# Performance work log

Measured on AMD Instinct MI355X. Metric: run time of the kernel, lower is better.

Reference implementation:

```python
import jax, jax.numpy as jnp
import numpy as np

QK_SCALE = 10.0  # fixed scale used with qk_norm (x-transformers/zeta default)
NEG_INF = -1e9


def layernorm(x, g, b, eps=1e-5):
    mu = jnp.mean(x, axis=-1, keepdims=True)
    var = jnp.var(x, axis=-1, keepdims=True)
    return (x - mu) * jax.lax.rsqrt(var + eps) * g + b


def l2norm(x, eps=1e-12):
    return x / jnp.sqrt(jnp.sum(x * x, axis=-1, keepdims=True) + eps)


def setup_inputs() -> dict:
    key = jax.random.key(0)
    ks = jax.random.split(key, 10)
    B, S, D, H, DH, E, FF = 2, 1024, 1024, 16, 64, 8, 4096
    sd = lambda fan: 1.0 / np.sqrt(fan)
    return {
        'x': jax.random.normal(ks[0], (B, S, D), jnp.float32),
        'ln_g': jnp.ones((D,), jnp.float32),
        'ln_b': jnp.zeros((D,), jnp.float32),
        'Wq': jax.random.normal(ks[1], (D, H * DH), jnp.float32) * sd(D),
        'Wk': jax.random.normal(ks[2], (D, H * DH), jnp.float32) * sd(D),
        'Wv': jax.random.normal(ks[3], (D, H * DH), jnp.float32) * sd(D),
        'q_scale': jnp.ones((H, 1, DH), jnp.float32),
        'k_scale': jnp.ones((H, 1, DH), jnp.float32),
        'Wo': jax.random.normal(ks[4], (H * DH, D), jnp.float32) * sd(H * DH),
        'gate_w': jax.random.normal(ks[5], (D, E), jnp.float32) * sd(D),
        'gate_b': jnp.zeros((E,), jnp.float32),
        'w1': jax.random.normal(ks[6], (E, D, FF), jnp.float32) * sd(D),
        'b1': jnp.zeros((E, FF), jnp.float32),
        'w2': jax.random.normal(ks[7], (E, FF, D), jnp.float32) * sd(FF),
        'b2': jnp.zeros((E, D), jnp.float32),
    }


def reference(x, ln_g, ln_b, Wq, Wk, Wv, q_scale, k_scale, Wo,
              gate_w, gate_b, w1, b1, w2, b2):
    B, S, D = x.shape
    H = q_scale.shape[0]
    DH = q_scale.shape[-1]

    # pre-attention LayerNorm (shared params)
    h = layernorm(x, ln_g, ln_b)

    # qk-normed causal multi-head attention
    q = (h @ Wq).reshape(B, S, H, DH).transpose(0, 2, 1, 3)  # b h s d
    k = (h @ Wk).reshape(B, S, H, DH).transpose(0, 2, 1, 3)
    v = (h @ Wv).reshape(B, S, H, DH).transpose(0, 2, 1, 3)
    q = l2norm(q) * q_scale
    k = l2norm(k) * k_scale
    logits = jnp.einsum('bhid,bhjd->bhij', q, k) * QK_SCALE
    causal = jnp.tril(jnp.ones((S, S), bool))
    logits = jnp.where(causal, logits, NEG_INF)
    attn = jax.nn.softmax(logits, axis=-1)
    out = jnp.einsum('bhij,bhjd->bhid', attn, v)
    out = out.transpose(0, 2, 1, 3).reshape(B, S, H * DH) @ Wo

    # mid LayerNorm (same shared params)
    h = layernorm(out, ln_g, ln_b)

    # SimpleMoE: softmax gate, dense combine over all experts
    gate = jax.nn.softmax(h @ gate_w + gate_b, axis=-1)  # b s e
    hid = jax.nn.gelu(jnp.einsum('bsd,edf->bsef', h, w1) + b1)  # b s e ff
    exp_out = jnp.einsum('bsef,efd->bsed', hid, w2) + b2  # b s e d
    moe = jnp.einsum('bse,bsed->bsd', gate, exp_out)

    # final LayerNorm (same shared params)
    return layernorm(moe, ln_g, ln_b)
```

## Files before the change

kernel.cpp:

```cpp
#include <hip/hip_runtime.h>

typedef unsigned short u16;
typedef float f32x4 __attribute__((ext_vector_type(4)));
typedef short short8 __attribute__((ext_vector_type(8)));

#define QK_SCALE_F 10.0f

#define GLD_LDS(g, l) __builtin_amdgcn_global_load_lds( \
    (const __attribute__((address_space(1))) unsigned int*)(g), \
    (__attribute__((address_space(3))) unsigned int*)(l), 16, 0, 0)

__device__ __forceinline__ u16 f2b(float f) {
  union { float f; unsigned u; } c; c.f = f;
  return (u16)((c.u + 0x7fffu + ((c.u >> 16) & 1u)) >> 16);
}

__device__ __forceinline__ float wred_sum(float v) {
#pragma unroll
  for (int m = 32; m > 0; m >>= 1) v += __shfl_xor(v, m, 64);
  return v;
}
__device__ __forceinline__ float wred_max(float v) {
#pragma unroll
  for (int m = 32; m > 0; m >>= 1) v = fmaxf(v, __shfl_xor(v, m, 64));
  return v;
}

#define BM 128
#define BN 128
#define BKK 64

template<int EPI>
__global__ __launch_bounds__(256)
void gemm_bt(const u16* __restrict__ A, const u16* __restrict__ B, void* __restrict__ Cv,
             int M, int N, int K, int lda, int ldb, int ldc,
             long zA, long zB, long zC,
             const float* __restrict__ P1, long zP1, const float* __restrict__ P2,
             int causal) {
  int z = blockIdx.z;
  int row0 = blockIdx.y * BM;
  int col0 = blockIdx.x * BN;
  if (causal && col0 > row0 + (BM - 1)) return;
  A += zA * z; B += zB * z;
  int tid = threadIdx.x;
  int wave = tid >> 6, lane = tid & 63;
  int wm = wave >> 1, wn = wave & 1;

  __shared__ __align__(16) u16 lA[2][BM * BKK];
  __shared__ __align__(16) u16 lB[2][BN * BKK];

  f32x4 acc[4][4];
  f32x4 zf = {0.f, 0.f, 0.f, 0.f};
#pragma unroll
  for (int i = 0; i < 4; i++)
#pragma unroll
    for (int j = 0; j < 4; j++) acc[i][j] = zf;

  int l3 = lane >> 3;
  int scol = ((lane & 7) ^ l3) << 3;
  long aoff[4], boff[4];
  int cbase[4];
#pragma unroll
  for (int i = 0; i < 4; i++) {
    int c = (wave << 2) + i;
    int r = (c << 3) + l3;
    aoff[i] = (long)(row0 + r) * lda + scol;
    boff[i] = (long)(col0 + r) * ldb + scol;
    cbase[i] = c << 10;
  }

  auto stage = [&](int buf, int k0) {
#pragma unroll
    for (int i = 0; i < 4; i++) {
      GLD_LDS(A + aoff[i] + k0, (char*)lA[buf] + cbase[i]);
      GLD_LDS(B + boff[i] + k0, (char*)lB[buf] + cbase[i]);
    }
  };

  int nt = K / BKK;
  stage(0, 0);
  int cur = 0;
  for (int t = 0; t < nt; ++t) {
    __syncthreads();
    if (t + 1 < nt) stage(cur ^ 1, (t + 1) * BKK);
    const char* pA = (const char*)lA[cur];
    const char* pB = (const char*)lB[cur];
#pragma unroll
    for (int kk = 0; kk < 2; kk++) {
      short8 af[4], bfr[4];
      int cb = (kk << 6) | ((lane >> 4) << 4);
#pragma unroll
      for (int mi = 0; mi < 4; mi++) {
        int R = (wm << 6) + (mi << 4) + (lane & 15);
        af[mi] = *(const short8*)(pA + ((R << 7) | (cb ^ ((R & 7) << 4))));
      }
#pragma unroll
      for (int nj = 0; nj < 4; nj++) {
        int R = (wn << 6) + (nj << 4) + (lane & 15);
        bfr[nj] = *(const short8*)(pB + ((R << 7) | (cb ^ ((R & 7) << 4))));
      }
#pragma unroll
      for (int mi = 0; mi < 4; mi++)
#pragma unroll
        for (int nj = 0; nj < 4; nj++)
          acc[mi][nj] = __builtin_amdgcn_mfma_f32_16x16x32_bf16(af[mi], bfr[nj], acc[mi][nj], 0, 0, 0);
    }
    cur ^= 1;
  }

#pragma unroll
  for (int mi = 0; mi < 4; mi++) {
#pragma unroll
    for (int nj = 0; nj < 4; nj++) {
#pragma unroll
      for (int rr = 0; rr < 4; rr++) {
        int row = row0 + (wm << 6) + (mi << 4) + ((lane >> 4) << 2) + rr;
        int col = col0 + (wn << 6) + (nj << 4) + (lane & 15);
        if (col < N) {
          float v = acc[mi][nj][rr];
          long cidx = zC * z + (long)row * ldc + col;
          if (EPI == 0) {
            ((float*)Cv)[cidx] = v;
          } else if (EPI == 2) {
            float t = v + P1[zP1 * z + col];
            float zz = 1.5957691216f * (t + 0.044715f * t * t * t);
            float gl = t / (1.f + __expf(-zz));
            ((u16*)Cv)[cidx] = f2b(gl * P2[((long)row << 3) + z]);
          }
        }
      }
    }
  }
}

__global__ __launch_bounds__(256)
void transpose_cast(const float* __restrict__ src, u16* __restrict__ dst,
                    int R, int C, long sz, long dz) {
  int z = blockIdx.z;
  src += sz * z; dst += dz * z;
  __shared__ float t[32][33];
  int c0 = blockIdx.x * 32, r0 = blockIdx.y * 32;
  int tx = threadIdx.x & 31, ty = threadIdx.x >> 5;
#pragma unroll
  for (int j = 0; j < 4; j++) {
    int r = ty + j * 8;
    t[r][tx] = src[(long)(r0 + r) * C + c0 + tx];
  }
  __syncthreads();
#pragma unroll
  for (int j = 0; j < 4; j++) {
    int r = ty + j * 8;
    dst[(long)(c0 + r) * R + r0 + tx] = f2b(t[tx][r]);
  }
}

__global__ __launch_bounds__(256)
void ln_kernel(const float* __restrict__ x, const float* __restrict__ g,
               const float* __restrict__ b, float* __restrict__ yf, u16* __restrict__ yb) {
  int tid = threadIdx.x;
  long base = (long)blockIdx.x << 10;
  float4 v = *(const float4*)&x[base + tid * 4];
  float s = v.x + v.y + v.z + v.w;
  float q = v.x * v.x + v.y * v.y + v.z * v.z + v.w * v.w;
  s = wred_sum(s); q = wred_sum(q);
  __shared__ float2 red[4];
  int wave = tid >> 6, lane = tid & 63;
  if (lane == 0) red[wave] = make_float2(s, q);
  __syncthreads();
  float S1 = red[0].x + red[1].x + red[2].x + red[3].x;
  float S2 = red[0].y + red[1].y + red[2].y + red[3].y;
  float mu = S1 * (1.f / 1024.f);
  float var = S2 * (1.f / 1024.f) - mu * mu;
  float rs = rsqrtf(var + 1e-5f);
  float4 gv = *(const float4*)&g[tid * 4];
  float4 bv = *(const float4*)&b[tid * 4];
  float4 o;
  o.x = (v.x - mu) * rs * gv.x + bv.x;
  o.y = (v.y - mu) * rs * gv.y + bv.y;
  o.z = (v.z - mu) * rs * gv.z + bv.z;
  o.w = (v.w - mu) * rs * gv.w + bv.w;
  if (yf) *(float4*)&yf[base + tid * 4] = o;
  if (yb) {
    ushort4 ob; ob.x = f2b(o.x); ob.y = f2b(o.y); ob.z = f2b(o.z); ob.w = f2b(o.w);
    *(ushort4*)&yb[base + tid * 4] = ob;
  }
}

__global__ __launch_bounds__(256)
void ln_reduce8(const float* __restrict__ sl, const float* __restrict__ gate,
                const float* __restrict__ b2, const float* __restrict__ g,
                const float* __restrict__ b, float* __restrict__ out) {
  int row = blockIdx.x, tid = threadIdx.x;
  __shared__ float gs[8];
  if (tid < 8) gs[tid] = gate[(row << 3) + tid];
  __syncthreads();
  long rbase = (long)row << 10;
  int col = tid << 2;
  float4 a = {0.f, 0.f, 0.f, 0.f};
#pragma unroll
  for (int s = 0; s < 8; s++) {
    float4 v = *(const float4*)&sl[(long)s * (2048l * 1024) + rbase + col];
    a.x += v.x; a.y += v.y; a.z += v.z; a.w += v.w;
  }
#pragma unroll
  for (int e = 0; e < 8; e++) {
    float4 bv = *(const float4*)&b2[(e << 10) + col];
    float ge = gs[e];
    a.x += ge * bv.x; a.y += ge * bv.y; a.z += ge * bv.z; a.w += ge * bv.w;
  }
  float s1 = a.x + a.y + a.z + a.w;
  float q = a.x * a.x + a.y * a.y + a.z * a.z + a.w * a.w;
  s1 = wred_sum(s1); q = wred_sum(q);
  __shared__ float2 red[4];
  int wave = tid >> 6, lane = tid & 63;
  if (lane == 0) red[wave] = make_float2(s1, q);
  __syncthreads();
  float S1 = red[0].x + red[1].x + red[2].x + red[3].x;
  float S2 = red[0].y + red[1].y + red[2].y + red[3].y;
  float mu = S1 * (1.f / 1024.f);
  float var = S2 * (1.f / 1024.f) - mu * mu;
  float rs = rsqrtf(var + 1e-5f);
  float4 gv = *(const float4*)&g[col];
  float4 bv = *(const float4*)&b[col];
  float4 o;
  o.x = (a.x - mu) * rs * gv.x + bv.x;
  o.y = (a.y - mu) * rs * gv.y + bv.y;
  o.z = (a.z - mu) * rs * gv.z + bv.z;
  o.w = (a.w - mu) * rs * gv.w + bv.w;
  *(float4*)&out[rbase + col] = o;
}

__global__ __launch_bounds__(256)
void l2norm_kernel(const float* __restrict__ src, const float* __restrict__ scale,
                   u16* __restrict__ dst, int ld, int off) {
  int r = blockIdx.x * 4 + (threadIdx.x >> 6);
  int lane = threadIdx.x & 63;
  float v = src[(long)(r >> 4) * ld + off + ((r & 15) << 6) + lane];
  float ss = v * v;
#pragma unroll
  for (int m = 32; m > 0; m >>= 1) ss += __shfl_xor(ss, m, 64);
  int h = r & 15, sIdx = (r >> 4) & 1023, b = r >> 14;
  float o = v * rsqrtf(ss + 1e-12f) * scale[(h << 6) + lane];
  dst[((((long)(b * 16 + h)) << 10) + sIdx) * 64 + lane] = f2b(o);
}

__global__ __launch_bounds__(256)
void v_transpose(const float* __restrict__ vf, u16* __restrict__ vT) {
  int z = blockIdx.x, b = z >> 4, h = z & 15, s0 = blockIdx.y * 16;
  __shared__ u16 t[64][17];
  int si = threadIdx.x >> 6, d = threadIdx.x & 63;
#pragma unroll
  for (int j = 0; j < 4; j++) {
    int sl = j * 4 + si;
    t[d][sl] = f2b(vf[((long)(b << 10) + (s0 + sl)) * 3072 + 2048 + (h << 6) + d]);
  }
  __syncthreads();
  int d2 = threadIdx.x >> 2, sj = threadIdx.x & 3;
#pragma unroll
  for (int j = 0; j < 4; j++) {
    int sl = j * 4 + sj;
    vT[((long)(z * 128 + d2) << 10) + s0 + sl] = t[d2][sl];
  }
}

__global__ __launch_bounds__(256)
void softmax_kernel(const float* __restrict__ logits, u16* __restrict__ P) {
  int i = blockIdx.x, z = blockIdx.y, tid = threadIdx.x;
  long base = ((long)z << 20) + ((long)i << 10);
  int len = i + 1;
  float lv[4];
  float mx = -1e30f;
  int cnt = 0;
  for (int j = tid; j < len; j += 256) { float l = logits[base + j] * QK_SCALE_F; lv[cnt++] = l; mx = fmaxf(mx, l); }
  mx = wred_max(mx);
  __shared__ float red[4];
  int wave = tid >> 6, lane = tid & 63;
  if (lane == 0) red[wave] = mx;
  __syncthreads();
  mx = fmaxf(fmaxf(red[0], red[1]), fmaxf(red[2], red[3]));
  float s = 0.f;
  for (int c = 0; c < cnt; c++) { lv[c] = __expf(lv[c] - mx); s += lv[c]; }
  s = wred_sum(s);
  __syncthreads();
  if (lane == 0) red[wave] = s;
  __syncthreads();
  s = red[0] + red[1] + red[2] + red[3];
  float inv = 1.f / s;
  cnt = 0;
  for (int j = tid; j < len; j += 256) P[base + j] = f2b(lv[cnt++] * inv);
  for (int j = tid; j < 1024; j += 256) if (j >= len) P[base + j] = 0;
}

__global__ __launch_bounds__(256)
void attn_cat_kernel(const float* __restrict__ pv, u16* __restrict__ acat) {
  int blk = blockIdx.x; int b = blk >> 10, i = blk & 1023;
#pragma unroll
  for (int j = 0; j < 4; ++j) {
    int col = threadIdx.x + j * 256;
    int h = col >> 6, d = col & 63;
    float v = pv[(((long)(b * 16 + h)) << 16) + (i << 6) + d];
    acat[((long)blk << 10) + col] = f2b(v);
  }
}

__global__ __launch_bounds__(256)
void gate_kernel(const float* __restrict__ h2, const float* __restrict__ gw,
                 const float* __restrict__ gb, float* __restrict__ gate) {
  int row = blockIdx.x, tid = threadIdx.x;
  const float* hr = h2 + ((long)row << 10);
  float acc[8];
#pragma unroll
  for (int e = 0; e < 8; e++) acc[e] = 0.f;
  for (int d = tid; d < 1024; d += 256) {
    float hv = hr[d];
    const float4* wp = (const float4*)&gw[d * 8];
    float4 w0 = wp[0], w1v = wp[1];
    acc[0] += hv * w0.x;  acc[1] += hv * w0.y;  acc[2] += hv * w0.z;  acc[3] += hv * w0.w;
    acc[4] += hv * w1v.x; acc[5] += hv * w1v.y; acc[6] += hv * w1v.z; acc[7] += hv * w1v.w;
  }
  __shared__ float red[8][4];
  int wave = tid >> 6, lane = tid & 63;
#pragma unroll
  for (int e = 0; e < 8; e++) { float v = wred_sum(acc[e]); if (lane == 0) red[e][wave] = v; }
  __syncthreads();
  if (tid == 0) {
    float l[8]; float mx = -1e30f;
    for (int e = 0; e < 8; e++) { l[e] = red[e][0] + red[e][1] + red[e][2] + red[e][3] + gb[e]; mx = fmaxf(mx, l[e]); }
    float s = 0.f;
    for (int e = 0; e < 8; e++) { l[e] = __expf(l[e] - mx); s += l[e]; }
    float inv = 1.f / s;
    for (int e = 0; e < 8; e++) gate[row * 8 + e] = l[e] * inv;
  }
}

extern "C" void kernel_launch(void* const* d_in, const int* in_sizes, int n_in,
                              void* d_out, int out_size, void* d_ws, size_t ws_size,
                              hipStream_t stream) {
  const float* x   = (const float*)d_in[0];
  const float* lng = (const float*)d_in[1];
  const float* lnb = (const float*)d_in[2];
  const float* Wq  = (const float*)d_in[3];
  const float* Wk  = (const float*)d_in[4];
  const float* Wv  = (const float*)d_in[5];
  const float* qs  = (const float*)d_in[6];
  const float* ks  = (const float*)d_in[7];
  const float* Wo  = (const float*)d_in[8];
  const float* gw  = (const float*)d_in[9];
  const float* gb  = (const float*)d_in[10];
  const float* w1  = (const float*)d_in[11];
  const float* b1  = (const float*)d_in[12];
  const float* w2  = (const float*)d_in[13];
  const float* b2  = (const float*)d_in[14];
  float* out = (float*)d_out;

  char* base = (char*)d_ws;
  size_t off = 0;
  auto alloc = [&](size_t bytes) { void* p = base + off; off = (off + bytes + 255) & ~(size_t)255; return p; };

  u16*   W1T  = (u16*)alloc(8l * 1024 * 4096 * 2);
  u16*   W2T  = (u16*)alloc(1024l * 32768 * 2);
  u16*   WQKVT= (u16*)alloc(3072l * 1024 * 2);
  u16*   WOT  = (u16*)alloc(1024l * 1024 * 2);
  u16*   HB   = (u16*)alloc(2048l * 1024 * 2);
  float* QKVF = (float*)alloc(2048l * 3072 * 4);
  u16*   QN   = (u16*)alloc(2048l * 1024 * 2);
  u16*   KN   = (u16*)alloc(2048l * 1024 * 2);
  u16*   VT   = (u16*)alloc(32l * 128 * 1024 * 2);
  float* LOG  = (float*)alloc(32l * 1024 * 1024 * 4);
  u16*   P    = (u16*)alloc(32l * 1024 * 1024 * 2);
  float* PV   = (float*)alloc(32l * 1024 * 64 * 4);
  u16*   ACAT = (u16*)alloc(2048l * 1024 * 2);
  float* APROJ= (float*)alloc(2048l * 1024 * 4);
  float* H2F  = (float*)alloc(2048l * 1024 * 4);
  u16*   H2B  = (u16*)alloc(2048l * 1024 * 2);
  float* GATE = (float*)alloc(2048l * 8 * 4);
  u16*   HID  = (u16*)LOG;
  float* MOE8 = (float*)P;

  if (off > ws_size) return;

  dim3 blk(256);

  transpose_cast<<<dim3(32, 32, 1), blk, 0, stream>>>(Wq, WQKVT, 1024, 1024, 0, 0);
  transpose_cast<<<dim3(32, 32, 1), blk, 0, stream>>>(Wk, WQKVT + 1024l * 1024, 1024, 1024, 0, 0);
  transpose_cast<<<dim3(32, 32, 1), blk, 0, stream>>>(Wv, WQKVT + 2048l * 1024, 1024, 1024, 0, 0);
  transpose_cast<<<dim3(32, 32, 1), blk, 0, stream>>>(Wo, WOT, 1024, 1024, 0, 0);
  transpose_cast<<<dim3(128, 32, 8), blk, 0, stream>>>(w1, W1T, 1024, 4096, 1024l * 4096, 4096l * 1024);
  transpose_cast<<<dim3(32, 1024, 1), blk, 0, stream>>>(w2, W2T, 32768, 1024, 0, 0);

  ln_kernel<<<2048, blk, 0, stream>>>(x, lng, lnb, nullptr, HB);

  gemm_bt<0><<<dim3(24, 16, 1), blk, 0, stream>>>(HB, WQKVT, QKVF, 2048, 3072, 1024, 1024, 1024, 3072,
                                                  0, 0, 0, nullptr, 0, nullptr, 0);

  l2norm_kernel<<<8192, blk, 0, stream>>>(QKVF, qs, QN, 3072, 0);
  l2norm_kernel<<<8192, blk, 0, stream>>>(QKVF, ks, KN, 3072, 1024);
  v_transpose<<<dim3(32, 64, 1), blk, 0, stream>>>(QKVF, VT);

  gemm_bt<0><<<dim3(8, 8, 32), blk, 0, stream>>>(QN, KN, LOG, 1024, 1024, 64, 64, 64, 1024,
                                                 65536, 65536, 1048576, nullptr, 0, nullptr, 1);
  softmax_kernel<<<dim3(1024, 32, 1), blk, 0, stream>>>(LOG, P);
  gemm_bt<0><<<dim3(1, 8, 32), blk, 0, stream>>>(P, VT, PV, 1024, 64, 1024, 1024, 1024, 64,
                                                 1048576, 131072, 65536, nullptr, 0, nullptr, 0);
  attn_cat_kernel<<<2048, blk, 0, stream>>>(PV, ACAT);

  gemm_bt<0><<<dim3(8, 16, 1), blk, 0, stream>>>(ACAT, WOT, APROJ, 2048, 1024, 1024, 1024, 1024, 1024,
                                                 0, 0, 0, nullptr, 0, nullptr, 0);
  ln_kernel<<<2048, blk, 0, stream>>>(APROJ, lng, lnb, H2F, H2B);

  gate_kernel<<<2048, blk, 0, stream>>>(H2F, gw, gb, GATE);
  gemm_bt<2><<<dim3(32, 16, 8), blk, 0, stream>>>(H2B, W1T, HID, 2048, 4096, 1024, 1024, 1024, 32768,
                                                  0, 4096l * 1024, 4096, b1, 4096, GATE, 0);
  gemm_bt<0><<<dim3(8, 16, 8), blk, 0, stream>>>(HID, W2T, MOE8, 2048, 1024, 4096, 32768, 32768, 1024,
                                                 4096, 4096, 2048l * 1024, nullptr, 0, nullptr, 0);

  ln_reduce8<<<2048, blk, 0, stream>>>(MOE8, GATE, b2, lng, lnb, out);
}
```

Before: 1.012 ms.

## Deepen GEMM LDS pipeline to four buffers with explicit vmcnt waits

The bf16 MFMA GEMM moves from a double-buffered LDS loop to a four-buffer ring that keeps three K-tiles of global_load_lds in flight. A hand-written s_waitcnt vmcnt plus s_barrier waits only for the oldest tile instead of draining all outstanding loads, so global-memory latency can overlap with more compute. The trade-off is that LDS use per block doubles, which likely cuts the number of resident blocks per CU and may offset the gain in latency hiding. A tail sequence handles the last tiles with decreasing vmcnt thresholds.

```diff
diff --git a/kernel.cpp b/kernel.cpp
--- a/kernel.cpp
+++ b/kernel.cpp
@@ -9,6 +9,8 @@
 #define GLD_LDS(g, l) __builtin_amdgcn_global_load_lds( \
     (const __attribute__((address_space(1))) unsigned int*)(g), \
     (__attribute__((address_space(3))) unsigned int*)(l), 16, 0, 0)
+
+#define WAITBAR(N) asm volatile("s_waitcnt vmcnt(" #N ")\ns_barrier" ::: "memory")
 
 __device__ __forceinline__ u16 f2b(float f) {
   union { float f; unsigned u; } c; c.f = f;
@@ -46,8 +48,8 @@
   int wave = tid >> 6, lane = tid & 63;
   int wm = wave >> 1, wn = wave & 1;
 
-  __shared__ __align__(16) u16 lA[2][BM * BKK];
-  __shared__ __align__(16) u16 lB[2][BN * BKK];
+  __shared__ __align__(16) u16 lA[4][BM * BKK];
+  __shared__ __align__(16) u16 lB[4][BN * BKK];
 
   f32x4 acc[4][4];
   f32x4 zf = {0.f, 0.f, 0.f, 0.f};
@@ -77,14 +79,9 @@
     }
   };
 
-  int nt = K / BKK;
-  stage(0, 0);
-  int cur = 0;
-  for (int t = 0; t < nt; ++t) {
-    __syncthreads();
-    if (t + 1 < nt) stage(cur ^ 1, (t + 1) * BKK);
-    const char* pA = (const char*)lA[cur];
-    const char* pB = (const char*)lB[cur];
+  auto compute = [&](int buf) {
+    const char* pA = (const char*)lA[buf];
+    const char* pB = (const char*)lB[buf];
 #pragma unroll
     for (int kk = 0; kk < 2; kk++) {
       short8 af[4], bfr[4];
@@ -105,7 +102,33 @@
         for (int nj = 0; nj < 4; nj++)
           acc[mi][nj] = __builtin_amdgcn_mfma_f32_16x16x32_bf16(af[mi], bfr[nj], acc[mi][nj], 0, 0, 0);
     }
-    cur ^= 1;
+  };
+
+  int nt = K / BKK;
+  stage(0, 0);
+  if (nt > 1) stage(1, BKK);
+  if (nt > 2) stage(2, 2 * BKK);
+  int t = 0;
+  for (; t + 3 < nt; ++t) {
+    WAITBAR(16);
+    stage((t + 3) & 3, (t + 3) * BKK);
+    compute(t & 3);
+  }
+  if (t < nt) {
+    int r = nt - t;
+    if (r == 3)      { WAITBAR(16); }
+    else if (r == 2) { WAITBAR(8); }
+    else             { WAITBAR(0); }
+    compute(t & 3); ++t;
+  }
+  if (t < nt) {
+    if (nt - t == 2) { WAITBAR(8); }
+    else             { WAITBAR(0); }
+    compute(t & 3); ++t;
+  }
+  if (t < nt) {
+    WAITBAR(0);
+    compute(t & 3); ++t;
   }
 
 #pragma unroll
@@ -122,9 +145,9 @@
           if (EPI == 0) {
             ((float*)Cv)[cidx] = v;
           } else if (EPI == 2) {
-            float t = v + P1[zP1 * z + col];
-            float zz = 1.5957691216f * (t + 0.044715f * t * t * t);
-            float gl = t / (1.f + __expf(-zz));
+            float tv = v + P1[zP1 * z + col];
+            float zz = 1.5957691216f * (tv + 0.044715f * tv * tv * tv);
+            float gl = tv / (1.f + __expf(-zz));
             ((u16*)Cv)[cidx] = f2b(gl * P2[((long)row << 3) + z]);
           }
         }
```

After: 1.388 ms. +37.1%, slower.

## Add 256x256-tile four-stage pipelined GEMM for MoE expert matmuls

Applied to the files above, without the earlier changes.

Adds a new 512-thread GEMM kernel with 256x256 output tiles, a 4-deep LDS ring buffer fed by global_load_lds, and explicit vmcnt waits plus barriers. The two MoE expert GEMMs, which dominate the FLOPs, now use it. The larger tile is meant to raise data reuse per byte loaded, and the deeper prefetch is meant to hide memory latency. The cost is heavier register and LDS use (128 KB of LDS per block requested with 2 blocks per CU), which risks spills or lower occupancy. The old GEMM loses its GELU epilogue.

```diff
diff --git a/kernel.cpp b/kernel.cpp
--- a/kernel.cpp
+++ b/kernel.cpp
@@ -10,6 +10,8 @@
     (const __attribute__((address_space(1))) unsigned int*)(g), \
     (__attribute__((address_space(3))) unsigned int*)(l), 16, 0, 0)
 
+#define WAITBAR(N) asm volatile("s_waitcnt vmcnt(" #N ")\ns_barrier" ::: "memory")
+
 __device__ __forceinline__ u16 f2b(float f) {
   union { float f; unsigned u; } c; c.f = f;
   return (u16)((c.u + 0x7fffu + ((c.u >> 16) & 1u)) >> 16);
@@ -35,7 +37,6 @@
 void gemm_bt(const u16* __restrict__ A, const u16* __restrict__ B, void* __restrict__ Cv,
              int M, int N, int K, int lda, int ldb, int ldc,
              long zA, long zB, long zC,
-             const float* __restrict__ P1, long zP1, const float* __restrict__ P2,
              int causal) {
   int z = blockIdx.z;
   int row0 = blockIdx.y * BM;
@@ -119,14 +120,108 @@
         if (col < N) {
           float v = acc[mi][nj][rr];
           long cidx = zC * z + (long)row * ldc + col;
-          if (EPI == 0) {
-            ((float*)Cv)[cidx] = v;
-          } else if (EPI == 2) {
-            float t = v + P1[zP1 * z + col];
-            float zz = 1.5957691216f * (t + 0.044715f * t * t * t);
-            float gl = t / (1.f + __expf(-zz));
-            ((u16*)Cv)[cidx] = f2b(gl * P2[((long)row << 3) + z]);
-          }
+          ((float*)Cv)[cidx] = v;
+        }
+      }
+    }
+  }
+}
+
+#define TBM 256
+#define TBN 256
+#define TBK 32
+
+template<int EPI>
+__global__ __launch_bounds__(512, 2)
+void gemm256(const u16* __restrict__ A, const u16* __restrict__ B, void* __restrict__ Cv,
+             int K, int lda, int ldb, int ldc,
+             long zA, long zB, long zC,
+             const float* __restrict__ P1, long zP1, const float* __restrict__ P2) {
+  int z = blockIdx.z;
+  int row0 = blockIdx.y * TBM;
+  int col0 = blockIdx.x * TBN;
+  A += zA * z; B += zB * z;
+  int tid = threadIdx.x;
+  int wave = tid >> 6, lane = tid & 63;
+  int wm = wave >> 2, wn = wave & 3;
+
+  __shared__ __align__(16) u16 lA[4][TBM * TBK];
+  __shared__ __align__(16) u16 lB[4][TBN * TBK];
+
+  f32x4 acc[8][4];
+  f32x4 zf = {0.f, 0.f, 0.f, 0.f};
+#pragma unroll
+  for (int i = 0; i < 8; i++)
+#pragma unroll
+    for (int j = 0; j < 4; j++) acc[i][j] = zf;
+
+  int r_in = tid >> 2;
+  int scol = (((tid & 3) ^ ((tid >> 3) & 3)) << 3);
+  long aoff0 = (long)(row0 + r_in) * lda + scol;
+  long aoff1 = (long)(row0 + 128 + r_in) * lda + scol;
+  long boff0 = (long)(col0 + r_in) * ldb + scol;
+  long boff1 = (long)(col0 + 128 + r_in) * ldb + scol;
+  int doff = tid << 4;
+
+  auto stage = [&](int buf, int kt) {
+    int k0 = kt * TBK;
+    GLD_LDS(A + aoff0 + k0, (char*)lA[buf] + doff);
+    GLD_LDS(A + aoff1 + k0, (char*)lA[buf] + 8192 + doff);
+    GLD_LDS(B + boff0 + k0, (char*)lB[buf] + doff);
+    GLD_LDS(B + boff1 + k0, (char*)lB[buf] + 8192 + doff);
+  };
+
+  auto compute = [&](int buf) {
+    const char* pA = (const char*)lA[buf];
+    const char* pB = (const char*)lB[buf];
+    int kb = (lane >> 4) << 4;
+    short8 af[8], bf[4];
+#pragma unroll
+    for (int m = 0; m < 8; m++) {
+      int R = (wm << 7) + (m << 4) + (lane & 15);
+      af[m] = *(const short8*)(pA + (R << 6) + (kb ^ (((R >> 1) & 3) << 4)));
+    }
+#pragma unroll
+    for (int n = 0; n < 4; n++) {
+      int R = (wn << 6) + (n << 4) + (lane & 15);
+      bf[n] = *(const short8*)(pB + (R << 6) + (kb ^ (((R >> 1) & 3) << 4)));
+    }
+#pragma unroll
+    for (int m = 0; m < 8; m++)
+#pragma unroll
+      for (int n = 0; n < 4; n++)
+        acc[m][n] = __builtin_amdgcn_mfma_f32_16x16x32_bf16(af[m], bf[n], acc[m][n], 0, 0, 0);
+  };
+
+  int nt = K / TBK;
+  stage(0, 0); stage(1, 1); stage(2, 2);
+  int t = 0;
+  for (; t + 3 < nt; ++t) {
+    WAITBAR(8);
+    stage((t + 3) & 3, t + 3);
+    compute(t & 3);
+  }
+  WAITBAR(8); compute(t & 3); ++t;
+  WAITBAR(4); compute(t & 3); ++t;
+  WAITBAR(0); compute(t & 3); ++t;
+
+#pragma unroll
+  for (int m = 0; m < 8; m++) {
+#pragma unroll
+    for (int n = 0; n < 4; n++) {
+#pragma unroll
+      for (int rr = 0; rr < 4; rr++) {
+        int row = row0 + (wm << 7) + (m << 4) + ((lane >> 4) << 2) + rr;
+        int col = col0 + (wn << 6) + (n << 4) + (lane & 15);
+        float v = acc[m][n][rr];
+        long cidx = zC * z + (long)row * ldc + col;
+        if (EPI == 0) {
+          ((float*)Cv)[cidx] = v;
+        } else {
+          float tv = v + P1[zP1 * z + col];
+          float zz = 1.5957691216f * (tv + 0.044715f * tv * tv * tv);
+          float gl = tv / (1.f + __expf(-zz));
+          ((u16*)Cv)[cidx] = f2b(gl * P2[((long)row << 3) + z]);
         }
       }
     }
@@ -391,28 +486,28 @@
   ln_kernel<<<2048, blk, 0, stream>>>(x, lng, lnb, nullptr, HB);
 
   gemm_bt<0><<<dim3(24, 16, 1), blk, 0, stream>>>(HB, WQKVT, QKVF, 2048, 3072, 1024, 1024, 1024, 3072,
-                                                  0, 0, 0, nullptr, 0, nullptr, 0);
+                                                  0, 0, 0, 0);
 
   l2norm_kernel<<<8192, blk, 0, stream>>>(QKVF, qs, QN, 3072, 0);
   l2norm_kernel<<<8192, blk, 0, stream>>>(QKVF, ks, KN, 3072, 1024);
   v_transpose<<<dim3(32, 64, 1), blk, 0, stream>>>(QKVF, VT);
 
   gemm_bt<0><<<dim3(8, 8, 32), blk, 0, stream>>>(QN, KN, LOG, 1024, 1024, 64, 64, 64, 1024,
-                                                 65536, 65536, 1048576, nullptr, 0, nullptr, 1);
+                                                 65536, 65536, 1048576, 1);
   softmax_kernel<<<dim3(1024, 32, 1), blk, 0, stream>>>(LOG, P);
   gemm_bt<0><<<dim3(1, 8, 32), blk, 0, stream>>>(P, VT, PV, 1024, 64, 1024, 1024, 1024, 64,
-                                                 1048576, 131072, 65536, nullptr, 0, nullptr, 0);
+                                                 1048576, 131072, 65536, 0);
   attn_cat_kernel<<<2048, blk, 0, stream>>>(PV, ACAT);
 
   gemm_bt<0><<<dim3(8, 16, 1), blk, 0, stream>>>(ACAT, WOT, APROJ, 2048, 1024, 1024, 1024, 1024, 1024,
-                                                 0, 0, 0, nullptr, 0, nullptr, 0);
+                                                 0, 0, 0, 0);
   ln_kernel<<<2048, blk, 0, stream>>>(APROJ, lng, lnb, H2F, H2B);
 
   gate_kernel<<<2048, blk, 0, stream>>>(H2F, gw, gb, GATE);
-  gemm_bt<2><<<dim3(32, 16, 8), blk, 0, stream>>>(H2B, W1T, HID, 2048, 4096, 1024, 1024, 1024, 32768,
-                                                  0, 4096l * 1024, 4096, b1, 4096, GATE, 0);
-  gemm_bt<0><<<dim3(8, 16, 8), blk, 0, stream>>>(HID, W2T, MOE8, 2048, 1024, 4096, 32768, 32768, 1024,
-                                                 4096, 4096, 2048l * 1024, nullptr, 0, nullptr, 0);
+  gemm256<2><<<dim3(16, 8, 8), dim3(512), 0, stream>>>(H2B, W1T, HID, 1024, 1024, 1024, 32768,
+                                                       0, 4096l * 1024, 4096, b1, 4096, GATE);
+  gemm256<0><<<dim3(4, 8, 8), dim3(512), 0, stream>>>(HID, W2T, MOE8, 4096, 32768, 32768, 1024,
+                                                      4096, 4096, 2048l * 1024, nullptr, 0, nullptr);
 
   ln_reduce8<<<2048, blk, 0, stream>>>(MOE8, GATE, b2, lng, lnb, out);
 }
```

Result: no change. 1.028 ms (+1.6%).
